# Kernel tuning notes

Measured on AMD Instinct MI355X. Metric: run time of the kernel, lower is better.

Reference implementation:

```python
import jax, jax.numpy as jnp
import numpy as np

BN_EPS = 1e-3  # keras BatchNormalization default epsilon


def _conv(x, w):
    # x: [B,H,W,Cin], w: [kh,kw,Cin,Cout], stride 1, SAME padding
    return jax.lax.conv_general_dilated(
        x, w, window_strides=(1, 1), padding='SAME',
        dimension_numbers=('NHWC', 'HWIO', 'NHWC'))


def _bn(x, g, b, m, v):
    return (x - m) * jax.lax.rsqrt(v + BN_EPS) * g + b


def _pam(x, wq, bq, wk, bk, wv, bv, gamma):
    # Position attention: softmax over HW x HW similarity of 1x1-conv q/k.
    B, H, W, C = x.shape
    q = (_conv(x, wq) + bq).reshape(B, H * W, -1)   # [B,HW,C/8]
    k = (_conv(x, wk) + bk).reshape(B, H * W, -1)   # [B,HW,C/8]
    v = (_conv(x, wv) + bv).reshape(B, H * W, C)    # [B,HW,C]
    energy = jnp.einsum('bic,bjc->bij', q, k)       # [B,HW,HW]
    att = jax.nn.softmax(energy, axis=-1)
    out = jnp.einsum('bij,bjc->bic', att, v).reshape(B, H, W, C)
    return gamma * out + x


def _cam(x, gamma):
    # Channel attention with max-subtract stabilization, softmax over C.
    B, H, W, C = x.shape
    X = x.reshape(B, H * W, C)                      # channel-last flat
    energy = jnp.einsum('bnc,bnd->bcd', X, X)       # [B,C,C]
    energy_new = jnp.max(energy, axis=-1, keepdims=True) - energy
    att = jax.nn.softmax(energy_new, axis=-1)       # [B,C,C]
    out = jnp.einsum('bcd,bnd->bnc', att, X).reshape(B, H, W, C)
    return gamma * out + x


def setup_inputs() -> dict:
    key = jax.random.key(0)
    ks = jax.random.split(key, 16)
    B, H, W = 4, 64, 64
    Cin, Ci, Cq, Cout = 512, 128, 16, 19
    s = 0.05
    d = {
        'x': jax.random.normal(ks[0], (B, H, W, Cin), jnp.float32),
        'w5a': jax.random.normal(ks[1], (3, 3, Cin, Ci), jnp.float32) * s,
        'w5c': jax.random.normal(ks[2], (3, 3, Cin, Ci), jnp.float32) * s,
        'wq': jax.random.normal(ks[3], (1, 1, Ci, Cq), jnp.float32) * s,
        'bq': jnp.zeros((Cq,), jnp.float32),
        'wk': jax.random.normal(ks[4], (1, 1, Ci, Cq), jnp.float32) * s,
        'bk': jnp.zeros((Cq,), jnp.float32),
        'wv': jax.random.normal(ks[5], (1, 1, Ci, Ci), jnp.float32) * s,
        'bv': jnp.zeros((Ci,), jnp.float32),
        'pam_gamma': jnp.float32(0.5),
        'cam_gamma': jnp.float32(0.5),
        'w51': jax.random.normal(ks[6], (3, 3, Ci, Ci), jnp.float32) * s,
        'w52': jax.random.normal(ks[7], (3, 3, Ci, Ci), jnp.float32) * s,
        'w8': jax.random.normal(ks[8], (1, 1, Ci, Cout), jnp.float32) * s,
    }
    for i, nm in enumerate(['bn1', 'bn2', 'bn3', 'bn4']):
        d[nm + '_g'] = jnp.ones((Ci,), jnp.float32)
        d[nm + '_b'] = jnp.zeros((Ci,), jnp.float32)
        d[nm + '_m'] = jax.random.normal(ks[9 + i], (Ci,), jnp.float32) * 0.1
        d[nm + '_v'] = jnp.ones((Ci,), jnp.float32)
    return d


def reference(x, w5a, w5c, wq, bq, wk, bk, wv, bv, pam_gamma, cam_gamma,
              w51, w52, w8,
              bn1_g, bn1_b, bn1_m, bn1_v,
              bn2_g, bn2_b, bn2_m, bn2_v,
              bn3_g, bn3_b, bn3_m, bn3_v,
              bn4_g, bn4_b, bn4_m, bn4_v):
    # PAM branch
    feat1 = jax.nn.relu(_bn(_conv(x, w5a), bn1_g, bn1_b, bn1_m, bn1_v))
    sa_feat = _pam(feat1, wq, bq, wk, bk, wv, bv, pam_gamma)
    sa_conv = jax.nn.relu(_bn(_conv(sa_feat, w51), bn3_g, bn3_b, bn3_m, bn3_v))
    # CAM branch
    feat2 = jax.nn.relu(_bn(_conv(x, w5c), bn2_g, bn2_b, bn2_m, bn2_v))
    sc_feat = _cam(feat2, cam_gamma)
    sc_conv = jax.nn.relu(_bn(_conv(sc_feat, w52), bn4_g, bn4_b, bn4_m, bn4_v))
    # Fused output (dropout is identity at inference)
    feat_sum = sa_conv + sc_conv
    return _conv(feat_sum, w8)
```

## Files before the change

kernel.cpp:

```cpp
#include <hip/hip_runtime.h>
#include <hip/hip_bf16.h>
#include <math.h>

#define BN_EPS 1e-3f
#define LOG2E 1.44269504088896f

constexpr int Bn = 4, Hn = 64, Wn = 64, CIN = 512, CI = 128;
constexpr int HWn = Hn * Wn;
constexpr int NPIX = Bn * HWn;
constexpr int COn = 19;
constexpr int XSL = 66;
constexpr int XPG = XSL * 16;

struct F8 { float4 lo, hi; };

__device__ __forceinline__ F8 f8zero() {
    F8 r; r.lo = make_float4(0.f,0.f,0.f,0.f); r.hi = make_float4(0.f,0.f,0.f,0.f); return r;
}
__device__ __forceinline__ void fma8(F8 &acc, float a, const float4 &wlo, const float4 &whi) {
    acc.lo.x = fmaf(a, wlo.x, acc.lo.x);
    acc.lo.y = fmaf(a, wlo.y, acc.lo.y);
    acc.lo.z = fmaf(a, wlo.z, acc.lo.z);
    acc.lo.w = fmaf(a, wlo.w, acc.lo.w);
    acc.hi.x = fmaf(a, whi.x, acc.hi.x);
    acc.hi.y = fmaf(a, whi.y, acc.hi.y);
    acc.hi.z = fmaf(a, whi.z, acc.hi.z);
    acc.hi.w = fmaf(a, whi.w, acc.hi.w);
}

typedef __attribute__((ext_vector_type(8)))  short    short8;
typedef __attribute__((ext_vector_type(8)))  _Float16 half8;
typedef __attribute__((ext_vector_type(16))) float    f32x16;

__device__ __forceinline__ f32x16 f16z() {
    f32x16 z;
    #pragma unroll
    for (int i = 0; i < 16; ++i) z[i] = 0.f;
    return z;
}
__device__ __forceinline__ unsigned f2b(float f) {
    union { float f; unsigned u; } c; c.f = f;
    return (c.u + 0x7FFFu + ((c.u >> 16) & 1u)) >> 16;
}
__device__ __forceinline__ unsigned pack2(float lo, float hi) {
    return (f2b(hi) << 16) | f2b(lo);
}
__device__ __forceinline__ unsigned pkb2(float a, float b) {
    __hip_bfloat16 ha = __float2bfloat16(a);
    __hip_bfloat16 hb = __float2bfloat16(b);
    return ((unsigned)*(unsigned short*)&hb << 16) | *(unsigned short*)&ha;
}
__device__ __forceinline__ void split2(float a, float b, unsigned &hi, unsigned &lo) {
    const unsigned ha = f2b(a), hb = f2b(b);
    union { unsigned u; float f; } ua, ub; ua.u = ha << 16; ub.u = hb << 16;
    hi = (hb << 16) | ha;
    lo = pack2(a - ua.f, b - ub.f);
}
__device__ __forceinline__ unsigned pkh2(float a, float b) {
    union { _Float16 h; unsigned short u; } ca, cb;
    ca.h = (_Float16)a; cb.h = (_Float16)b;
    return ((unsigned)cb.u << 16) | ca.u;
}

__global__ __launch_bounds__(256)
void k_prep_w(const float* __restrict__ w5a, const float* __restrict__ w5c,
              const float* __restrict__ w51, const float* __restrict__ w52,
              char* __restrict__ wt1F, char* __restrict__ wt2aF, char* __restrict__ wt2bF)
{
    int idx = blockIdx.x * 256 + threadIdx.x;
    if (idx < 589824) {
        const int jp = idx & 7, co = (idx >> 3) & 255, ct = idx >> 11;
        const int tap = ct % 9, c = ct / 9;
        const float* src = (co < 128) ? w5a : w5c;
        const int coc = co & 127;
        const int ci = c*16 + jp*2;
        const float a = src[((size_t)tap*CIN + ci)*CI + coc];
        const float b = src[((size_t)tap*CIN + ci + 1)*CI + coc];
        const int L = co*32 + jp*4;
        *(unsigned*)(wt1F + (size_t)ct*8192 + L) = pkh2(a, b);
    } else {
        int k = idx - 589824;
        if (k >= 147456) return;
        const float* src = (k < 73728) ? w51 : w52;
        char* dstF = (k < 73728) ? wt2aF : wt2bF;
        if (k >= 73728) k -= 73728;
        const int jp = k & 7, co = (k >> 3) & 127, ct = k >> 10;
        const int tap = ct % 9, c = ct / 9;
        const int ci = c*16 + jp*2;
        const float a = src[((size_t)tap*CI + ci)*CI + co];
        const float b = src[((size_t)tap*CI + ci + 1)*CI + co];
        const int L = co*32 + jp*4;
        *(unsigned*)(dstF + (size_t)ct*4096 + L) = pkh2(a, b);
    }
}

__global__ __launch_bounds__(256)
void k_prep_bn(const float* g1, const float* b1, const float* m1, const float* v1,
               const float* g2, const float* b2, const float* m2, const float* v2,
               const float* g3, const float* b3, const float* m3, const float* v3,
               const float* g4, const float* b4, const float* m4, const float* v4,
               float* bnAs, float* bnAb, float* bnBs, float* bnBb)
{
    const int t = threadIdx.x, c = t & 127;
    {
        const float *g = (t < 128) ? g1 : g2, *b = (t < 128) ? b1 : b2;
        const float *m = (t < 128) ? m1 : m2, *v = (t < 128) ? v1 : v2;
        const float s = g[c] * rsqrtf(v[c] + BN_EPS);
        bnAs[t] = s; bnAb[t] = b[c] - m[c]*s;
    }
    {
        const float *g = (t < 128) ? g3 : g4, *b = (t < 128) ? b3 : b4;
        const float *m = (t < 128) ? m3 : m4, *v = (t < 128) ? v3 : v4;
        const float s = g[c] * rsqrtf(v[c] + BN_EPS);
        bnBs[t] = s; bnBb[t] = b[c] - m[c]*s;
    }
}

__global__ __launch_bounds__(256)
void k_prep_x(const float* __restrict__ x, _Float16* __restrict__ xcv)
{
    __shared__ float Xl[16*520];
    const int t = threadIdx.x;
    const int pb = blockIdx.x * 16;
    #pragma unroll
    for (int i = 0; i < 8; ++i) {
        const int u = t + i*256;
        const int px = u >> 7, c4 = (u & 127) * 4;
        *(float4*)&Xl[px*520 + c4] = *(const float4*)&x[(size_t)(pb + px)*CIN + c4];
    }
    __syncthreads();
    const int rowg = pb >> 6, pixb = pb & 63;
    #pragma unroll
    for (int i = 0; i < 8; ++i) {
        const int u = t + i*256;
        const int chunk = u >> 6, rem = u & 63;
        const int pl = rem >> 2, u4 = rem & 3;
        const float* src = &Xl[pl*520 + chunk*16 + u4*4];
        uint2 v;
        v.x = pkh2(src[0], src[1]);
        v.y = pkh2(src[2], src[3]);
        *(uint2*)&xcv[(((size_t)rowg*32 + chunk)*XSL + (pixb + pl + 1))*16 + u4*4] = v;
    }
    if (pixb == 0 && t < 64) {
        const int chunk = t >> 1, sl = (t & 1) * 65;
        uint4* dst = (uint4*)&xcv[(((size_t)rowg*32 + chunk)*XSL + sl)*16];
        uint4 z; z.x = 0u; z.y = 0u; z.z = 0u; z.w = 0u;
        dst[0] = z; dst[1] = z;
    }
}

__global__ __launch_bounds__(256)
void k_zhalo(_Float16* __restrict__ saf_h, _Float16* __restrict__ scf_h)
{
    const int idx = blockIdx.x * 256 + threadIdx.x;
    if (idx >= 8192) return;
    _Float16* arr = (idx & 4096) ? scf_h : saf_h;
    const int rem = idx & 4095;
    const int row = rem >> 4, chunk = (rem >> 1) & 7, sl = (rem & 1) * 65;
    uint4* dst = (uint4*)&arr[(((size_t)row*8 + chunk)*XSL + sl)*16];
    uint4 z; z.x = 0u; z.y = 0u; z.z = 0u; z.w = 0u;
    dst[0] = z; dst[1] = z;
}

template<int NCHNK, int NCOTOT, int WCOBASE>
__global__ __launch_bounds__(256)
void k_convg(const _Float16* __restrict__ xcv0, const _Float16* __restrict__ xcv1,
             const _Float16* __restrict__ wtF0, const _Float16* __restrict__ wtF1,
             const float* __restrict__ bnS, const float* __restrict__ bnBi,
             float* __restrict__ out0, float* __restrict__ out1)
{
    const int t    = threadIdx.x;
    const int wgid = blockIdx.x;
    const int xcd  = wgid & 7;
    const int sel  = xcd >> 2;
    const int ch2  = (xcd >> 1) & 1;
    const int row  = ((wgid >> 3) << 1) | (xcd & 1);
    const _Float16* xcv = sel ? xcv1 : xcv0;
    const _Float16* wtF = sel ? wtF1 : wtF0;
    float* dst = sel ? out1 : out0;

    const int hh = row & 63;
    const int dyLo = (hh == 0)  ? 1 : 0;
    const int dyHi = (hh == 63) ? 1 : 2;
    const int l = t & 63, w = t >> 6;
    const int lo5 = l & 31, hf = l >> 5;
    const int mi = w >> 1, nt = w & 1;
    const int corow = WCOBASE*sel + ch2*64 + nt*32 + lo5;

    unsigned xbase[3];
    #pragma unroll
    for (int dy = 0; dy < 3; ++dy)
        xbase[dy] = (unsigned)(((row + dy - 1)*NCHNK)*XPG + (mi*32 + lo5)*16 + hf*8);
    const unsigned wbase = (unsigned)(corow*16 + hf*8);

    f32x16 acc = f16z();

    #pragma unroll 2
    for (int c = 0; c < NCHNK; ++c) {
        #pragma unroll
        for (int dy = 0; dy < 3; ++dy) {
            if (dy < dyLo || dy > dyHi) continue;
            half8 wf[3], xf[3];
            #pragma unroll
            for (int dx = 0; dx < 3; ++dx) {
                wf[dx] = *(const half8*)&wtF[(size_t)((c*9 + dy*3 + dx)*NCOTOT)*16 + wbase];
                xf[dx] = *(const half8*)&xcv[(size_t)xbase[dy] + (size_t)c*XPG + dx*16];
            }
            #pragma unroll
            for (int dx = 0; dx < 3; ++dx)
                acc = __builtin_amdgcn_mfma_f32_32x32x16_f16(wf[dx], xf[dx], acc, 0, 0, 0);
        }
    }
    const int px = mi*32 + lo5;
    const size_t pg = (size_t)row*Wn + px;
    #pragma unroll
    for (int r = 0; r < 16; ++r) {
        const int crow = (r & 3) + 8*(r >> 2) + 4*hf;
        const int och = ch2*64 + nt*32 + crow;
        const int bnidx = sel*128 + och;
        dst[pg*CI + och] = fmaxf(fmaf(acc[r], bnS[bnidx], bnBi[bnidx]), 0.f);
    }
}

__global__ __launch_bounds__(256)
void k_qk(const float* __restrict__ feat1,
          const float* __restrict__ wq, const float* __restrict__ bq,
          const float* __restrict__ wk, const float* __restrict__ bk,
          __hip_bfloat16* __restrict__ qb, __hip_bfloat16* __restrict__ kb)
{
    __shared__ float Al[64*129];
    __shared__ __align__(16) float Wl[128*32];
    const int t = threadIdx.x;
    const int pb = blockIdx.x * 64;
    for (int idx = t; idx < 64*128; idx += 256) {
        const int p = idx >> 7, ci = idx & 127;
        Al[p*129 + ci] = feat1[(size_t)(pb + p)*CI + ci];
    }
    for (int idx = t; idx < 128*32; idx += 256) {
        const int ci = idx >> 5, c = idx & 31;
        Wl[idx] = (c < 16) ? wq[ci*16 + c] : wk[ci*16 + (c - 16)];
    }
    __syncthreads();
    const int p = t & 63, cg = t >> 6, co = cg * 8;
    F8 acc = f8zero();
    #pragma unroll 8
    for (int ci = 0; ci < 128; ++ci) {
        const float a = Al[p*129 + ci];
        const float4 wlo = *(const float4*)&Wl[ci*32 + co];
        const float4 whi = *(const float4*)&Wl[ci*32 + co + 4];
        fma8(acc, a, wlo, whi);
    }
    const float* af = (const float*)&acc;
    #pragma unroll
    for (int j = 0; j < 8; ++j) {
        const int c = co + j;
        if (c < 16) qb[(size_t)(pb + p)*16 + c]        = __float2bfloat16((af[j] + bq[c]) * LOG2E);
        else        kb[(size_t)(pb + p)*16 + (c - 16)] = __float2bfloat16(af[j] + bk[c - 16]);
    }
}

__global__ __launch_bounds__(256)
void k_v(const float* __restrict__ feat1, const float* __restrict__ wv,
         const float* __restrict__ bv, __hip_bfloat16* __restrict__ vbT)
{
    __shared__ float Al[32*129];
    __shared__ __align__(16) float Wl[64*128];
    const int t = threadIdx.x;
    const int pb = blockIdx.x * 32;
    for (int idx = t; idx < 32*128; idx += 256) {
        const int p = idx >> 7, ci = idx & 127;
        Al[p*129 + ci] = feat1[(size_t)(pb + p)*CI + ci];
    }
    const int px = t & 15, co = (t >> 4) * 8;
    F8 acc0 = f8zero(), acc1 = f8zero();
    for (int ch = 0; ch < 2; ++ch) {
        __syncthreads();
        #pragma unroll
        for (int r = 0; r < 8; ++r) {
            const int i4 = t + r*256;
            const int kk = i4 >> 5, c4 = (i4 & 31) * 4;
            *(float4*)&Wl[kk*128 + c4] = *(const float4*)&wv[(size_t)(ch*64 + kk)*CI + c4];
        }
        __syncthreads();
        #pragma unroll 4
        for (int kk = 0; kk < 64; ++kk) {
            const float a0 = Al[px*129 + ch*64 + kk];
            const float a1 = Al[(px+16)*129 + ch*64 + kk];
            const float4 wlo = *(const float4*)&Wl[kk*128 + co];
            const float4 whi = *(const float4*)&Wl[kk*128 + co + 4];
            fma8(acc0, a0, wlo, whi);
            fma8(acc1, a1, wlo, whi);
        }
    }
    const int p0 = pb + px;
    const int bb = p0 / HWn, pin0 = p0 % HWn;
    const int k16a = pin0 >> 4, ko = pin0 & 15;
    const float* a0f = (const float*)&acc0;
    const float* a1f = (const float*)&acc1;
    #pragma unroll
    for (int j = 0; j < 8; ++j) {
        const int c = co + j;
        const size_t base = ((size_t)bb*256*CI*16) + (size_t)c*16 + ko;
        vbT[base + (size_t)k16a*CI*16]       = __float2bfloat16(a0f[j] + bv[c]);
        vbT[base + (size_t)(k16a + 1)*CI*16] = __float2bfloat16(a1f[j] + bv[c]);
    }
}

__global__ __launch_bounds__(256)
void k_pam(const __hip_bfloat16* __restrict__ qb, const __hip_bfloat16* __restrict__ kb,
           const __hip_bfloat16* __restrict__ vbT, const float* __restrict__ feat1,
           const float* __restrict__ gamma, _Float16* __restrict__ saf_h)
{
    __shared__ __align__(16) char pbuf[16896];
    __shared__ float msArr[4][32];
    __shared__ float ssArr[4][32];
    __shared__ float ssum[32];
    const int t  = threadIdx.x;
    const int wv = t >> 6, l = t & 63;
    const int lo5 = l & 31, h = l >> 5;
    unsigned* Ppk = (unsigned*)(pbuf + wv*4096);
    float* osum = (float*)pbuf;

    const int q0 = blockIdx.x * 32;
    const int bb = q0 / HWn;
    const size_t jb = (size_t)bb * HWn;
    const __hip_bfloat16* vbB = vbT + (size_t)bb * 256 * CI * 16;

    const short8 qfrag = *(const short8*)&qb[(size_t)(q0 + lo5)*16 + 8*h];
    const f32x16 zro = f16z();

    f32x16 o[4];
    #pragma unroll
    for (int cb = 0; cb < 4; ++cb) o[cb] = f16z();

    float m_run = -1e30f, s_run = 0.f;

    for (int k0 = wv*1024; k0 < wv*1024 + 1024; k0 += 64) {
        const short8 kf0 = *(const short8*)&kb[(jb + k0 +      lo5)*16 + 8*h];
        const short8 kf1 = *(const short8*)&kb[(jb + k0 + 32 + lo5)*16 + 8*h];
        short8 vf[4][4];
        #pragma unroll
        for (int s = 0; s < 4; ++s)
            #pragma unroll
            for (int cb = 0; cb < 4; ++cb)
                vf[s][cb] = *(const short8*)&vbB[
                    (((size_t)(k0 >> 4) + s)*CI + cb*32 + lo5)*16 + 8*h];

        f32x16 e0 = __builtin_amdgcn_mfma_f32_32x32x16_bf16(kf0, qfrag, zro, 0, 0, 0);
        f32x16 e1 = __builtin_amdgcn_mfma_f32_32x32x16_bf16(kf1, qfrag, zro, 0, 0, 0);

        float mt = fmaxf(e0[0], e1[0]);
        #pragma unroll
        for (int r = 1; r < 16; ++r) mt = fmaxf(mt, fmaxf(e0[r], e1[r]));
        mt = fmaxf(mt, __shfl_xor(mt, 32));

        if (__any(mt > m_run + 11.5416f)) {
            const float mnew = fmaxf(m_run, mt);
            const float sc = exp2f(m_run - mnew);
            s_run *= sc;
            #pragma unroll
            for (int cb = 0; cb < 4; ++cb)
                #pragma unroll
                for (int r = 0; r < 16; ++r) o[cb][r] *= sc;
            m_run = mnew;
        }

        #pragma unroll
        for (int r = 0; r < 16; ++r) {
            e0[r] = exp2f(e0[r] - m_run);
            e1[r] = exp2f(e1[r] - m_run);
        }
        float ss = 0.f;
        #pragma unroll
        for (int r = 0; r < 16; ++r) ss += e0[r] + e1[r];
        s_run += ss;

        #pragma unroll
        for (int r = 0; r < 16; r += 2) {
            const int pidx = ((r & 3) >> 1) + 4*(r >> 2) + 2*h;
            Ppk[pidx*32 + lo5]        = pkb2(e0[r], e0[r+1]);
            Ppk[(16 + pidx)*32 + lo5] = pkb2(e1[r], e1[r+1]);
        }
        #pragma unroll
        for (int s = 0; s < 4; ++s) {
            union { unsigned u[4]; short8 s8; } P;
            #pragma unroll
            for (int w = 0; w < 4; ++w)
                P.u[w] = Ppk[(s*8 + 4*h + w)*32 + lo5];
            #pragma unroll
            for (int cb = 0; cb < 4; ++cb)
                o[cb] = __builtin_amdgcn_mfma_f32_32x32x16_bf16(vf[s][cb], P.s8, o[cb], 0, 0, 0);
        }
    }

    const float s_w = s_run + __shfl_xor(s_run, 32);
    if (h == 0) { msArr[wv][lo5] = m_run; ssArr[wv][lo5] = s_w; }
    __syncthreads();

    float M = msArr[0][lo5];
    #pragma unroll
    for (int w = 1; w < 4; ++w) M = fmaxf(M, msArr[w][lo5]);
    float stot = 0.f;
    #pragma unroll
    for (int w = 0; w < 4; ++w) stot += exp2f(msArr[w][lo5] - M) * ssArr[w][lo5];
    if (wv == 0 && h == 0) ssum[lo5] = stot;
    const float myscale = exp2f(m_run - M);
    #pragma unroll
    for (int cb = 0; cb < 4; ++cb)
        #pragma unroll
        for (int r = 0; r < 16; ++r) o[cb][r] *= myscale;

    for (int w = 0; w < 4; ++w) {
        if (wv == w) {
            #pragma unroll
            for (int cb = 0; cb < 4; ++cb)
                #pragma unroll
                for (int r = 0; r < 16; ++r) {
                    const int c = cb*32 + (r & 3) + 8*(r >> 2) + 4*h;
                    float* p = &osum[lo5*132 + c];
                    if (w == 0) *p = o[cb][r]; else *p += o[cb][r];
                }
        }
        __syncthreads();
    }

    const float g = gamma[0];
    const int qloc = t >> 3, ch8 = t & 7;
    const float inv = 1.f / ssum[qloc];
    const int pgl = q0 + qloc;
    const int rowp = pgl >> 6, pixp = pgl & 63;
    const size_t gbase = (size_t)pgl*CI + ch8*16;
    union { _Float16 hv[16]; uint4 u[2]; } tmp;
    #pragma unroll
    for (int j = 0; j < 16; ++j)
        tmp.hv[j] = (_Float16)(g*(osum[qloc*132 + ch8*16 + j]*inv) + feat1[gbase + j]);
    uint4* dsth = (uint4*)&saf_h[(((size_t)rowp*8 + ch8)*XSL + (pixp + 1))*16];
    dsth[0] = tmp.u[0];
    dsth[1] = tmp.u[1];
}

__global__ __launch_bounds__(256)
void k_xpose(const float* __restrict__ feat2,
             char* __restrict__ f2TH, char* __restrict__ f2TL)
{
    __shared__ float Xl[64*129];
    const int t = threadIdx.x;
    const int pb = blockIdx.x * 64;
    const int bb = pb / HWn, pin = pb % HWn;
    for (int idx = t; idx < 64*128; idx += 256) {
        const int p = idx >> 7, ci = idx & 127;
        Xl[p*129 + ci] = feat2[(size_t)(pb + p)*CI + ci];
    }
    __syncthreads();
    const int c = t >> 1, half = t & 1;
    const size_t rowb = ((size_t)(bb*CI + c)*HWn + pin + half*32) * 2;
    #pragma unroll
    for (int j = 0; j < 16; ++j) {
        const float a = Xl[(half*32 + 2*j)*129 + c];
        const float b = Xl[(half*32 + 2*j + 1)*129 + c];
        unsigned hi, lo; split2(a, b, hi, lo);
        *(unsigned*)(f2TH + rowb + 4*j) = hi;
        *(unsigned*)(f2TL + rowb + 4*j) = lo;
    }
}

__global__ __launch_bounds__(256)
void k_cam_energy_m(const char* __restrict__ f2TH, const char* __restrict__ f2TL,
                    float* __restrict__ epart)
{
    __shared__ __align__(16) char Vh[128*256];
    __shared__ __align__(16) char Vl[128*256];
    const int t = threadIdx.x;
    const int ks = blockIdx.x, bb = blockIdx.y;
    const int l = t & 63, w = t >> 6;
    const int lo5 = l & 31, hf = l >> 5;

    #pragma unroll
    for (int pass = 0; pass < 8; ++pass) {
        const int slot = pass*256 + t;
        const int c = slot >> 4, g = slot & 15;
        const size_t gaddr = ((size_t)(bb*CI + c)*HWn + ks*128)*2 + g*16;
        const int laddr = c*256 + ((g*16) ^ ((c & 15) << 4));
        *(float4*)(Vh + laddr) = *(const float4*)(f2TH + gaddr);
        *(float4*)(Vl + laddr) = *(const float4*)(f2TL + gaddr);
    }
    __syncthreads();

    f32x16 acc[4];
    #pragma unroll
    for (int nj = 0; nj < 4; ++nj) acc[nj] = f16z();
    const int cA = w*32 + lo5;
    const int swA = (cA & 15) << 4;

    #pragma unroll
    for (int kk = 0; kk < 8; ++kk) {
        const int kb = kk*32 + hf*16;
        const short8 ah = *(const short8*)(Vh + cA*256 + (kb ^ swA));
        const short8 al = *(const short8*)(Vl + cA*256 + (kb ^ swA));
        #pragma unroll
        for (int nj = 0; nj < 4; ++nj) {
            const int dB = nj*32 + lo5;
            const int swB = (dB & 15) << 4;
            const short8 bh = *(const short8*)(Vh + dB*256 + (kb ^ swB));
            const short8 bl = *(const short8*)(Vl + dB*256 + (kb ^ swB));
            acc[nj] = __builtin_amdgcn_mfma_f32_32x32x16_bf16(ah, bh, acc[nj], 0, 0, 0);
            acc[nj] = __builtin_amdgcn_mfma_f32_32x32x16_bf16(al, bh, acc[nj], 0, 0, 0);
            acc[nj] = __builtin_amdgcn_mfma_f32_32x32x16_bf16(ah, bl, acc[nj], 0, 0, 0);
        }
    }
    float* ep = epart + ((size_t)(bb*32 + ks)*CI)*CI;
    #pragma unroll
    for (int nj = 0; nj < 4; ++nj)
        #pragma unroll
        for (int r = 0; r < 16; ++r) {
            const int c = w*32 + (r & 3) + 8*(r >> 2) + 4*hf;
            ep[(size_t)c*CI + nj*32 + lo5] = acc[nj][r];
        }
}

__global__ __launch_bounds__(64)
void k_cam_rs(const float* __restrict__ epart, float* __restrict__ att)
{
    const int lane = threadIdx.x;
    const int row = blockIdx.x;
    const int bb = row >> 7, c = row & 127;
    float2 e = make_float2(0.f, 0.f);
    for (int ks = 0; ks < 32; ++ks) {
        const float2 v = *(const float2*)&epart[
            ((size_t)(bb*32 + ks)*CI + c)*CI + lane*2];
        e.x += v.x; e.y += v.y;
    }
    float M = fmaxf(e.x, e.y);
    #pragma unroll
    for (int off = 32; off > 0; off >>= 1) M = fmaxf(M, __shfl_xor(M, off));
    const float en0 = M - e.x, en1 = M - e.y;
    float mx = fmaxf(en0, en1);
    #pragma unroll
    for (int off = 32; off > 0; off >>= 1) mx = fmaxf(mx, __shfl_xor(mx, off));
    const float p0 = __expf(en0 - mx), p1 = __expf(en1 - mx);
    float s = p0 + p1;
    #pragma unroll
    for (int off = 32; off > 0; off >>= 1) s += __shfl_xor(s, off);
    const float inv = 1.f / s;
    float2 o; o.x = p0*inv; o.y = p1*inv;
    *(float2*)&att[(size_t)row*CI + lane*2] = o;
}

__global__ __launch_bounds__(256)
void k_cam_apply(const float* __restrict__ feat2, const float* __restrict__ att,
                 const float* __restrict__ gamma, _Float16* __restrict__ scf_h)
{
    __shared__ float Xl[64*129];
    __shared__ __align__(16) float aT[128*64];
    const int t = threadIdx.x;
    const int pb = blockIdx.x * 64;
    const int bb = pb / HWn;
    const int ch = blockIdx.y * 64;
    for (int idx = t; idx < 64*128; idx += 256) {
        const int p = idx >> 7, ci = idx & 127;
        Xl[p*129 + ci] = feat2[(size_t)(pb + p)*CI + ci];
    }
    for (int idx = t; idx < 128*64; idx += 256) {
        const int d = idx >> 6, cc = idx & 63;
        aT[d*64 + cc] = att[((size_t)bb*CI + ch + cc)*CI + d];
    }
    __syncthreads();
    const int px = t & 63, cg = t >> 6;
    F8 accA = f8zero(), accB = f8zero();
    #pragma unroll 4
    for (int d = 0; d < 128; ++d) {
        const float xv = Xl[px*129 + d];
        const float* ap = &aT[d*64 + cg*16];
        const float4 a0 = *(const float4*)&ap[0];
        const float4 a1 = *(const float4*)&ap[4];
        const float4 a2 = *(const float4*)&ap[8];
        const float4 a3 = *(const float4*)&ap[12];
        fma8(accA, xv, a0, a1);
        fma8(accB, xv, a2, a3);
    }
    const float g = gamma[0];
    const float* fa = (const float*)&accA;
    const float* fb = (const float*)&accB;
    const int p0g = pb + px;
    const int rowA = p0g >> 6, pixA = p0g & 63;
    const int chunkA = (ch >> 4) + cg;
    const size_t baseA = (((size_t)rowA*8 + chunkA)*XSL + (pixA + 1))*16;
    #pragma unroll
    for (int j = 0; j < 8; ++j) {
        const int cA = ch + cg*16 + j;
        const int cB = cA + 8;
        scf_h[baseA + j]     = (_Float16)(g*fa[j] + Xl[px*129 + cA]);
        scf_h[baseA + 8 + j] = (_Float16)(g*fb[j] + Xl[px*129 + cB]);
    }
}

__global__ __launch_bounds__(256)
void k_final(const float* __restrict__ sa, const float* __restrict__ sc,
             const float* __restrict__ w8, float* __restrict__ out)
{
    __shared__ float Xl[64*129];
    __shared__ float w8l[128*COn];
    const int t = threadIdx.x;
    const int pb = blockIdx.x * 64;
    for (int idx = t; idx < 64*128; idx += 256) {
        const int p = idx >> 7, ci = idx & 127;
        const size_t gi = (size_t)(pb + p)*CI + ci;
        Xl[p*129 + ci] = sa[gi] + sc[gi];
    }
    for (int idx = t; idx < 128*COn; idx += 256) w8l[idx] = w8[idx];
    __syncthreads();
    for (int idx = t; idx < 64*COn; idx += 256) {
        const int p = idx / COn, co = idx - p*COn;
        float acc = 0.f;
        #pragma unroll 8
        for (int ci = 0; ci < 128; ++ci)
            acc = fmaf(Xl[p*129 + ci], w8l[ci*COn + co], acc);
        out[(size_t)(pb + p)*COn + co] = acc;
    }
}

extern "C" void kernel_launch(void* const* d_in, const int* in_sizes, int n_in,
                              void* d_out, int out_size, void* d_ws, size_t ws_size,
                              hipStream_t stream)
{
    const float* x    = (const float*)d_in[0];
    const float* w5a  = (const float*)d_in[1];
    const float* w5c  = (const float*)d_in[2];
    const float* wq   = (const float*)d_in[3];
    const float* bq   = (const float*)d_in[4];
    const float* wk   = (const float*)d_in[5];
    const float* bk   = (const float*)d_in[6];
    const float* wv   = (const float*)d_in[7];
    const float* bv   = (const float*)d_in[8];
    const float* pgam = (const float*)d_in[9];
    const float* cgam = (const float*)d_in[10];
    const float* w51  = (const float*)d_in[11];
    const float* w52  = (const float*)d_in[12];
    const float* w8   = (const float*)d_in[13];
    const float* bn1g = (const float*)d_in[14];
    const float* bn1b = (const float*)d_in[15];
    const float* bn1m = (const float*)d_in[16];
    const float* bn1v = (const float*)d_in[17];
    const float* bn2g = (const float*)d_in[18];
    const float* bn2b = (const float*)d_in[19];
    const float* bn2m = (const float*)d_in[20];
    const float* bn2v = (const float*)d_in[21];
    const float* bn3g = (const float*)d_in[22];
    const float* bn3b = (const float*)d_in[23];
    const float* bn3m = (const float*)d_in[24];
    const float* bn3v = (const float*)d_in[25];
    const float* bn4g = (const float*)d_in[26];
    const float* bn4b = (const float*)d_in[27];
    const float* bn4m = (const float*)d_in[28];
    const float* bn4v = (const float*)d_in[29];

    char* wsb = (char*)d_ws;
    float* feat1 = (float*)(wsb + 0);
    char*  f2TH  = wsb + 0;
    char*  f2TL  = wsb + 4194304;
    float* feat2 = (float*)(wsb + 8388608);
    _Float16* xcv   = (_Float16*)(wsb + 16777216);
    _Float16* saf_h = (_Float16*)(wsb + 16777216);
    _Float16* scf_h = (_Float16*)(wsb + 21102592);
    float*    epart = (float*)(wsb + 25427968);
    float* att = (float*)(wsb + 33816576);
    __hip_bfloat16* qb16 = (__hip_bfloat16*)(wsb + 34078720);
    __hip_bfloat16* kb16 = (__hip_bfloat16*)(wsb + 34603008);
    __hip_bfloat16* vbT  = (__hip_bfloat16*)(wsb + 35127296);
    char* wt1F  = wsb + 39321600;
    char* wt2aF = wsb + 41680896;
    char* wt2bF = wsb + 41975808;
    float* bnAs = (float*)(wsb + 42270720);
    float* bnAb = (float*)(wsb + 42271744);
    float* bnBs = (float*)(wsb + 42272768);
    float* bnBb = (float*)(wsb + 42273792);
    float* sa_conv = feat1;
    float* sc_conv = feat2;
    float* out  = (float*)d_out;

    k_prep_w<<<dim3(2880), 256, 0, stream>>>(w5a, w5c, w51, w52, wt1F, wt2aF, wt2bF);
    k_prep_bn<<<dim3(1), 256, 0, stream>>>(bn1g, bn1b, bn1m, bn1v, bn2g, bn2b, bn2m, bn2v,
                                           bn3g, bn3b, bn3m, bn3v, bn4g, bn4b, bn4m, bn4v,
                                           bnAs, bnAb, bnBs, bnBb);
    k_prep_x<<<dim3(1024), 256, 0, stream>>>(x, xcv);
    k_convg<32, 256, 128><<<dim3(1024), 256, 0, stream>>>(
        xcv, xcv, (const _Float16*)wt1F, (const _Float16*)wt1F, bnAs, bnAb, feat1, feat2);
    k_zhalo<<<dim3(32), 256, 0, stream>>>(saf_h, scf_h);
    k_qk<<<dim3(NPIX/64), 256, 0, stream>>>(feat1, wq, bq, wk, bk, qb16, kb16);
    k_v<<<dim3(NPIX/32), 256, 0, stream>>>(feat1, wv, bv, vbT);
    k_pam<<<dim3(NPIX/32), 256, 0, stream>>>(qb16, kb16, vbT, feat1, pgam, saf_h);
    k_xpose<<<dim3(NPIX/64), 256, 0, stream>>>(feat2, f2TH, f2TL);
    k_cam_energy_m<<<dim3(32, Bn), 256, 0, stream>>>(f2TH, f2TL, epart);
    k_cam_rs<<<dim3(Bn*CI), 64, 0, stream>>>(epart, att);
    k_cam_apply<<<dim3(NPIX/64, 2), 256, 0, stream>>>(feat2, att, cgam, scf_h);
    k_convg<8, 128, 0><<<dim3(1024), 256, 0, stream>>>(
        saf_h, scf_h, (const _Float16*)wt2aF, (const _Float16*)wt2bF,
        bnBs, bnBb, sa_conv, sc_conv);
    k_final<<<dim3(NPIX/64), 256, 0, stream>>>(sa_conv, sc_conv, w8, out);
}
```

Before: 243.3 us.

## Stage conv weights and input rows through double-buffered LDS with register prefetch

```diff
diff --git a/kernel.cpp b/kernel.cpp
--- a/kernel.cpp
+++ b/kernel.cpp
@@ -164,11 +164,16 @@
 
 template<int NCHNK, int NCOTOT, int WCOBASE>
 __global__ __launch_bounds__(256)
-void k_convg(const _Float16* __restrict__ xcv0, const _Float16* __restrict__ xcv1,
+void k_convl(const _Float16* __restrict__ xcv0, const _Float16* __restrict__ xcv1,
              const _Float16* __restrict__ wtF0, const _Float16* __restrict__ wtF1,
              const float* __restrict__ bnS, const float* __restrict__ bnBi,
              float* __restrict__ out0, float* __restrict__ out1)
 {
+    constexpr int WU4  = 1152;
+    constexpr int XU4  = 396;
+    constexpr int BUFB = (WU4 + XU4) * 16;
+    __shared__ __align__(16) char Ls[2*BUFB];
+
     const int t    = threadIdx.x;
     const int wgid = blockIdx.x;
     const int xcd  = wgid & 7;
@@ -185,31 +190,70 @@
     const int l = t & 63, w = t >> 6;
     const int lo5 = l & 31, hf = l >> 5;
     const int mi = w >> 1, nt = w & 1;
-    const int corow = WCOBASE*sel + ch2*64 + nt*32 + lo5;
-
-    unsigned xbase[3];
-    #pragma unroll
-    for (int dy = 0; dy < 3; ++dy)
-        xbase[dy] = (unsigned)(((row + dy - 1)*NCHNK)*XPG + (mi*32 + lo5)*16 + hf*8);
-    const unsigned wbase = (unsigned)(corow*16 + hf*8);
+    const int cobase0 = WCOBASE*sel + ch2*64;
+
+    bool sAct[7]; bool sIsW[7]; int sDst[7]; unsigned sSrc[7]; unsigned sStr[7];
+    #pragma unroll
+    for (int i = 0; i < 7; ++i) {
+        const int u = t + i*256;
+        sAct[i] = false; sIsW[i] = false; sDst[i] = -1; sSrc[i] = 0; sStr[i] = 0;
+        if (u < WU4) {
+            const int tap = u >> 7, rem = u & 127;
+            sAct[i] = true; sIsW[i] = true;
+            sSrc[i] = (unsigned)((tap*NCOTOT + cobase0)*32 + rem*16);
+            sStr[i] = (unsigned)(9*NCOTOT*32);
+            sDst[i] = (tap*128 + (rem & 1)*64 + (rem >> 1)) * 16;
+        } else if (u < WU4 + XU4) {
+            const int j = u - WU4;
+            const int page = j / 132, rem132 = j - page*132;
+            const int slot = rem132 >> 1, u4h = rem132 & 1;
+            sAct[i] = (page >= dyLo && page <= dyHi);
+            sSrc[i] = (unsigned)((((row + page - 1)*NCHNK)*XPG + slot*16 + u4h*8) * 2);
+            sStr[i] = (unsigned)(XPG*2);
+            sDst[i] = (WU4 + j) * 16;
+        }
+    }
+    int xoff[3];
+    #pragma unroll
+    for (int dx = 0; dx < 3; ++dx)
+        xoff[dx] = WU4*16 + ((mi*32 + lo5 + dx)*2 + hf)*16;
+    const int wlane = (hf*64 + nt*32 + lo5)*16;
 
     f32x16 acc = f16z();
 
-    #pragma unroll 2
+    uint4 xr[7];
+    auto loadS = [&](int c) {
+        #pragma unroll
+        for (int i = 0; i < 7; ++i) {
+            uint4 v; v.x = 0u; v.y = 0u; v.z = 0u; v.w = 0u;
+            if (sAct[i]) {
+                const char* base = sIsW[i] ? (const char*)wtF : (const char*)xcv;
+                v = *(const uint4*)(base + (size_t)sSrc[i] + (size_t)c*sStr[i]);
+            }
+            xr[i] = v;
+        }
+    };
+
+    loadS(0);
+    int p = 0;
     for (int c = 0; c < NCHNK; ++c) {
+        char* Lp = Ls + p*BUFB;
+        #pragma unroll
+        for (int i = 0; i < 7; ++i)
+            if (sDst[i] >= 0) *(uint4*)(Lp + sDst[i]) = xr[i];
+        __syncthreads();
+        if (c + 1 < NCHNK) loadS(c + 1);
         #pragma unroll
         for (int dy = 0; dy < 3; ++dy) {
             if (dy < dyLo || dy > dyHi) continue;
-            half8 wf[3], xf[3];
             #pragma unroll
             for (int dx = 0; dx < 3; ++dx) {
-                wf[dx] = *(const half8*)&wtF[(size_t)((c*9 + dy*3 + dx)*NCOTOT)*16 + wbase];
-                xf[dx] = *(const half8*)&xcv[(size_t)xbase[dy] + (size_t)c*XPG + dx*16];
+                const half8 wf = *(const half8*)(Lp + ((dy*3 + dx)*128)*16 + wlane);
+                const half8 xf = *(const half8*)(Lp + dy*(132*16) + xoff[dx]);
+                acc = __builtin_amdgcn_mfma_f32_32x32x16_f16(wf, xf, acc, 0, 0, 0);
             }
-            #pragma unroll
-            for (int dx = 0; dx < 3; ++dx)
-                acc = __builtin_amdgcn_mfma_f32_32x32x16_f16(wf[dx], xf[dx], acc, 0, 0, 0);
-        }
+        }
+        p ^= 1;
     }
     const int px = mi*32 + lo5;
     const size_t pg = (size_t)row*Wn + px;
@@ -683,7 +727,7 @@
                                            bn3g, bn3b, bn3m, bn3v, bn4g, bn4b, bn4m, bn4v,
                                            bnAs, bnAb, bnBs, bnBb);
     k_prep_x<<<dim3(1024), 256, 0, stream>>>(x, xcv);
-    k_convg<32, 256, 128><<<dim3(1024), 256, 0, stream>>>(
+    k_convl<32, 256, 128><<<dim3(1024), 256, 0, stream>>>(
         xcv, xcv, (const _Float16*)wt1F, (const _Float16*)wt1F, bnAs, bnAb, feat1, feat2);
     k_zhalo<<<dim3(32), 256, 0, stream>>>(saf_h, scf_h);
     k_qk<<<dim3(NPIX/64), 256, 0, stream>>>(feat1, wq, bq, wk, bk, qb16, kb16);
@@ -693,7 +737,7 @@
     k_cam_energy_m<<<dim3(32, Bn), 256, 0, stream>>>(f2TH, f2TL, epart);
     k_cam_rs<<<dim3(Bn*CI), 64, 0, stream>>>(epart, att);
     k_cam_apply<<<dim3(NPIX/64, 2), 256, 0, stream>>>(feat2, att, cgam, scf_h);
-    k_convg<8, 128, 0><<<dim3(1024), 256, 0, stream>>>(
+    k_convl<8, 128, 0><<<dim3(1024), 256, 0, stream>>>(
         saf_h, scf_h, (const _Float16*)wt2aF, (const _Float16*)wt2bF,
         bnBs, bnBb, sa_conv, sc_conv);
     k_final<<<dim3(NPIX/64), 256, 0, stream>>>(sa_conv, sc_conv, w8, out);
```

Result: no change. 244.2 us (+0.4%).
